# Kernel tuning notes

Measured on AMD Instinct MI355X. Metric: run time of the kernel, lower is better.

## Reference

```python
import jax, jax.numpy as jnp
import numpy as np

RADIUS = 0.1
NSAMPLE = 32


def _ball_query(radius, nsample, xyz, new_xyz):
    # xyz: (B,N,3), new_xyz: (B,npoint,3) -> idx (B,npoint,nsample) int32
    # Faithful to the CUDA ball_query: take the first nsample in-radius indices
    # (in ascending point order); pad with the first found index.
    N = xyz.shape[1]
    d2 = jnp.sum((new_xyz[:, :, None, :] - xyz[:, None, :, :]) ** 2, axis=-1)  # (B,np,N)
    mask = d2 < radius * radius
    key_arr = jnp.where(mask, jnp.arange(N, dtype=jnp.int32), jnp.int32(N))
    idx = jnp.sort(key_arr, axis=-1)[..., :nsample]  # (B,np,ns)
    first = idx[..., :1]
    idx = jnp.where(idx == N, first, idx)
    idx = jnp.where(idx == N, 0, idx)  # empty-ball fallback (matches zero-init buffer)
    return idx


def _group(features, idx):
    # features (B,C,N), idx (B,np,ns) -> (B,C,np,ns)
    return jax.vmap(lambda f, i: f[:, i])(features, idx)


def _forward(xyz, new_xyz):
    idx = jax.lax.stop_gradient(_ball_query(RADIUS, NSAMPLE, xyz, new_xyz))
    xyz_t = jnp.transpose(xyz, (0, 2, 1))                 # (B,3,N)
    g = _group(xyz_t, idx)                                # (B,3,np,ns) grouped_xyz
    c = jnp.transpose(new_xyz, (0, 2, 1))[..., None]      # (B,3,np,1)  new_xyz_reshaped

    # pairwise distances within each group
    diff = g[..., :, None] - g[..., None, :]              # (B,3,np,ns,ns)
    dis = jnp.sqrt(jnp.sum(diff * diff, axis=1))          # (B,np,ns,ns)
    mean_dis = jnp.mean(dis, axis=3)                      # (B,np,ns)
    tip_idx = jnp.argmax(mean_dis, axis=2)                # (B,np)
    tip_pts = jnp.take_along_axis(g, tip_idx[:, None, :, None], axis=3)[..., 0]  # (B,3,np)

    cb = jnp.broadcast_to(c, g.shape)                     # (B,3,np,ns)
    gpv = jnp.cross(jnp.cross(cb, g, axis=1), cb, axis=1)
    gpv = gpv / jnp.linalg.norm(gpv, axis=1)[:, None]     # (B,3,np,ns)

    new_r = jnp.sqrt(jnp.sum(c * c, axis=1))              # (B,np,1)
    new_norm = c / (new_r[:, None] + 1e-8)                # (B,3,np,1)

    c3 = c[..., 0]                                        # (B,3,np)
    tpv = jnp.cross(jnp.cross(c3, tip_pts, axis=1), c3, axis=1)
    tpv = tpv / jnp.linalg.norm(tpv, axis=1)[:, None]     # (B,3,np)

    gcv = jnp.cross(gpv, jnp.broadcast_to(tpv[..., None], gpv.shape), axis=1)
    sinv = jnp.sum(gcv * new_norm, axis=1)                # (B,np,ns)

    dis_t = jnp.transpose(dis, (0, 2, 1, 3))              # (B,ns,np,ns)
    dis_sort = jnp.sort(dis_t, axis=1) * sinv[:, None]    # (B,ns,np,ns)
    grouped_r = jnp.sqrt(jnp.sum(g * g, axis=1))          # (B,np,ns)
    return jnp.concatenate([dis_sort, grouped_r[:, None]], axis=1)  # (B,ns+1,np,ns)


def setup_inputs() -> dict:
    key = jax.random.key(0)
    k1, k2 = jax.random.split(key)
    xyz = jax.random.uniform(k1, (4, 16384, 3), dtype=jnp.float32)
    new_xyz = jax.random.uniform(k2, (4, 2048, 3), dtype=jnp.float32)
    return {"xyz": xyz, "new_xyz": new_xyz}


def reference(xyz, new_xyz):
    return _forward(xyz, new_xyz)
```

## Files before the change

kernel.cpp:

```cpp
#include <hip/hip_runtime.h>


#define BB 4
#define NN 16384
#define MM 2048
#define NS 32
#define R2 0.01f
#define NCELL 1000
#define CPAD 1024
#define HCAP 128

#define WS_PTS_OFF (16 * 1024)
#define WS_NEED (WS_PTS_OFF + (size_t)BB * NN * 16)

__device__ __forceinline__ int cell_of(float x, float y, float z) {
    int ci = (int)(x * 10.0f); ci = ci < 0 ? 0 : (ci > 9 ? 9 : ci);
    int cj = (int)(y * 10.0f); cj = cj < 0 ? 0 : (cj > 9 ? 9 : cj);
    int ck = (int)(z * 10.0f); ck = ck < 0 ? 0 : (ck > 9 ? 9 : ck);
    return (ci * 10 + cj) * 10 + ck;
}

__global__ __launch_bounds__(1024) void k_build(const float* __restrict__ xyz,
                                                int* __restrict__ off,
                                                float4* __restrict__ pts) {
    __shared__ int sc[1024];
    __shared__ int wsum[16];
    const int b = blockIdx.x, t = threadIdx.x;
    const int lane = t & 63, wid = t >> 6;
    sc[t] = 0;
    __syncthreads();
    const float* xp = xyz + (size_t)b * NN * 3;
    float X[16], Y[16], Z[16]; int C[16];
    #pragma unroll
    for (int k = 0; k < 16; ++k) {
        int i = k * 1024 + t;
        const float* p = xp + (size_t)i * 3;
        X[k] = p[0]; Y[k] = p[1]; Z[k] = p[2];
        C[k] = cell_of(X[k], Y[k], Z[k]);
        atomicAdd(&sc[C[k]], 1);
    }
    __syncthreads();
    int v = sc[t];
    int x = v;
    #pragma unroll
    for (int o = 1; o < 64; o <<= 1) {
        int u = __shfl_up(x, o);
        if (lane >= o) x += u;
    }
    if (lane == 63) wsum[wid] = x;
    __syncthreads();
    int pre = 0;
    #pragma unroll
    for (int i2 = 0; i2 < 16; ++i2) pre += (i2 < wid) ? wsum[i2] : 0;
    int incl = x + pre;
    int excl = incl - v;
    if (t < NCELL) off[b * CPAD + t] = excl;
    if (t == 1023) off[b * CPAD + NCELL] = incl;
    __syncthreads();
    sc[t] = excl;
    __syncthreads();
    #pragma unroll
    for (int k = 0; k < 16; ++k) {
        int pos = atomicAdd(&sc[C[k]], 1);
        int i = k * 1024 + t;
        pts[(size_t)b * NN + pos] = make_float4(X[k], Y[k], Z[k], __int_as_float(i));
    }
}

__global__ __launch_bounds__(256) void qgr_grid_kernel(
    const float* __restrict__ xyz,
    const float* __restrict__ nxyz,
    const int* __restrict__ offi,
    const float4* __restrict__ pts,
    float* __restrict__ out) {

    __shared__ float s_hx[4][2][HCAP], s_hy[4][2][HCAP], s_hz[4][2][HCAP];
    __shared__ int   s_hidx[4][2][HCAP];

    const int lane = threadIdx.x & 63;
    const int w = threadIdx.x >> 6;
    const int sub = lane & 31;
    const int half = lane >> 5;
    const int q0 = blockIdx.x * 8 + w * 2;
    const int b = q0 >> 11;

    const float* xb = xyz + (size_t)b * NN * 3;
    const float* nq = nxyz + (size_t)q0 * 3;
    const float cx0 = nq[0], cy0 = nq[1], cz0 = nq[2];
    const float cx1 = nq[3], cy1 = nq[4], cz1 = nq[5];
    const unsigned long long lmask = (1ull << lane) - 1ull;

    const int* offb = offi + b * CPAD;
    const float4* ptsb = pts + (size_t)b * NN;

    int hits01[2];
    for (int tq = 0; tq < 2; ++tq) {
        const float ccx = tq ? cx1 : cx0;
        const float ccy = tq ? cy1 : cy0;
        const float ccz = tq ? cz1 : cz0;

        int ci0 = (int)(ccx * 10.0f); ci0 = ci0 < 0 ? 0 : (ci0 > 9 ? 9 : ci0);
        int cj0 = (int)(ccy * 10.0f); cj0 = cj0 < 0 ? 0 : (cj0 > 9 ? 9 : cj0);
        int ck0 = (int)(ccz * 10.0f); ck0 = ck0 < 0 ? 0 : (ck0 > 9 ? 9 : ck0);
        int zlo = ck0 > 0 ? ck0 - 1 : 0;
        int zhi = ck0 < 9 ? ck0 + 1 : 9;

        int rs[9], rl[9];
        #pragma unroll
        for (int r = 0; r < 9; ++r) { rs[r] = 0; rl[r] = 0; }
        int nr = 0;
        #pragma unroll
        for (int di = -1; di <= 1; ++di) {
            int ii = ci0 + di; if ((unsigned)ii > 9u) continue;
            #pragma unroll
            for (int dj = -1; dj <= 1; ++dj) {
                int jj = cj0 + dj; if ((unsigned)jj > 9u) continue;
                int base2 = (ii * 10 + jj) * 10;
                int s0 = offb[base2 + zlo];
                int e0 = offb[base2 + zhi + 1];
                int len = e0 - s0;
                if (len > 0) { rs[nr] = s0; rl[nr] = len; ++nr; }
            }
        }

        float4 P[9];
        #pragma unroll
        for (int r = 0; r < 9; ++r) {
            int a = (lane < rl[r]) ? (rs[r] + lane) : 0;
            P[r] = ptsb[a];
        }

        int hits = 0;
        #pragma unroll
        for (int r = 0; r < 9; ++r) {
            float dx = __fsub_rn(ccx, P[r].x);
            float dy = __fsub_rn(ccy, P[r].y);
            float dz = __fsub_rn(ccz, P[r].z);
            float d2 = __fadd_rn(__fadd_rn(__fmul_rn(dx, dx), __fmul_rn(dy, dy)),
                                 __fmul_rn(dz, dz));
            bool hit = (lane < rl[r]) && (d2 < R2);
            unsigned long long bal = __ballot(hit);
            if (bal) {
                int rank = __popcll(bal & lmask);
                int slot = hits + rank;
                if (hit && slot < HCAP) {
                    s_hx[w][tq][slot] = P[r].x; s_hy[w][tq][slot] = P[r].y;
                    s_hz[w][tq][slot] = P[r].z; s_hidx[w][tq][slot] = __float_as_int(P[r].w);
                }
                hits += __popcll(bal);
            }
        }
        for (int r = 0; r < nr; ++r) {
            for (int t0 = 64; t0 < rl[r]; t0 += 64) {
                int t = t0 + lane;
                bool act = t < rl[r];
                float4 Q = ptsb[rs[r] + (act ? t : 0)];
                float dx = __fsub_rn(ccx, Q.x);
                float dy = __fsub_rn(ccy, Q.y);
                float dz = __fsub_rn(ccz, Q.z);
                float d2 = __fadd_rn(__fadd_rn(__fmul_rn(dx, dx), __fmul_rn(dy, dy)),
                                     __fmul_rn(dz, dz));
                bool hit = act && (d2 < R2);
                unsigned long long bal = __ballot(hit);
                if (bal) {
                    int rank = __popcll(bal & lmask);
                    int slot = hits + rank;
                    if (hit && slot < HCAP) {
                        s_hx[w][tq][slot] = Q.x; s_hy[w][tq][slot] = Q.y;
                        s_hz[w][tq][slot] = Q.z; s_hidx[w][tq][slot] = __float_as_int(Q.w);
                    }
                    hits += __popcll(bal);
                }
            }
        }
        hits01[tq] = hits;
    }

    const int hits = half ? hits01[1] : hits01[0];
    const int cap = hits < HCAP ? hits : HCAP;
    const float ccx = half ? cx1 : cx0;
    const float ccy = half ? cy1 : cy0;
    const float ccz = half ? cz1 : cz0;

    int key[4];
    #pragma unroll
    for (int r = 0; r < 4; ++r) {
        int e = r * 32 + sub;
        key[r] = (e < cap) ? ((s_hidx[w][half][e] << 8) | e) : 0x7fffffff;
    }

    #pragma unroll
    for (int k = 2; k <= 16; k <<= 1) {
        #pragma unroll
        for (int j = k >> 1; j > 0; j >>= 1) {
            bool lower = (sub & j) == 0;
            bool asc = (sub & k) == 0;
            bool keepmin = (lower == asc);
            #pragma unroll
            for (int r = 0; r < 4; ++r) {
                int p = __shfl_xor(key[r], j);
                key[r] = keepmin ? min(key[r], p) : max(key[r], p);
            }
        }
    }
    #pragma unroll
    for (int j = 16; j > 0; j >>= 1) {
        bool lower = (sub & j) == 0;
        #pragma unroll
        for (int r = 0; r < 4; ++r) {
            int p = __shfl_xor(key[r], j);
            bool asc = (r & 1) == 0;
            key[r] = (lower == asc) ? min(key[r], p) : max(key[r], p);
        }
    }
    {
        int t0 = min(key[0], key[1]); key[1] = max(key[0], key[1]); key[0] = t0;
        int t2 = max(key[2], key[3]); key[3] = min(key[2], key[3]); key[2] = t2;
    }
    #pragma unroll
    for (int j = 16; j > 0; j >>= 1) {
        bool lower = (sub & j) == 0;
        #pragma unroll
        for (int r = 0; r < 4; ++r) {
            int p = __shfl_xor(key[r], j);
            bool asc = (r & 2) == 0;
            key[r] = (lower == asc) ? min(key[r], p) : max(key[r], p);
        }
    }
    {
        int t0 = min(key[0], key[2]); key[2] = max(key[0], key[2]); key[0] = t0;
        int t1 = min(key[1], key[3]); key[3] = max(key[1], key[3]); key[1] = t1;
        t0 = min(key[0], key[1]); key[1] = max(key[0], key[1]); key[0] = t0;
        t1 = min(key[2], key[3]); key[3] = max(key[2], key[3]); key[2] = t1;
    }
    #pragma unroll
    for (int j = 16; j > 0; j >>= 1) {
        bool lower = (sub & j) == 0;
        #pragma unroll
        for (int r = 0; r < 4; ++r) {
            int p = __shfl_xor(key[r], j);
            key[r] = lower ? min(key[r], p) : max(key[r], p);
        }
    }

    const int found = hits < NS ? hits : NS;
    const int hbase = half << 5;
    float hx = 0.f, hy = 0.f, hz = 0.f;
    if (sub < found) {
        int s = key[0] & 0xFF;
        hx = s_hx[w][half][s]; hy = s_hy[w][half][s]; hz = s_hz[w][half][s];
    }
    float p0x, p0y, p0z;
    if (found == 0) { p0x = xb[0]; p0y = xb[1]; p0z = xb[2]; }
    else { p0x = __shfl(hx, hbase); p0y = __shfl(hy, hbase); p0z = __shfl(hz, hbase); }
    if (sub >= found) { hx = p0x; hy = p0y; hz = p0z; }

    float v[NS];
    #pragma unroll
    for (int ii = 0; ii < NS; ++ii) {
        float bx = __shfl(hx, hbase + ii);
        float by = __shfl(hy, hbase + ii);
        float bz = __shfl(hz, hbase + ii);
        float dx = __fsub_rn(bx, hx);
        float dy = __fsub_rn(by, hy);
        float dz = __fsub_rn(bz, hz);
        v[ii] = sqrtf(__fadd_rn(__fadd_rn(__fmul_rn(dx, dx), __fmul_rn(dy, dy)),
                                __fmul_rn(dz, dz)));
    }

    float r8[8];
    #pragma unroll
    for (int t = 0; t < 8; ++t) {
        r8[t] = __fadd_rn(__fadd_rn(__fadd_rn(v[t], v[t + 8]), v[t + 16]), v[t + 24]);
    }
    float mv = __fadd_rn(__fadd_rn(__fadd_rn(r8[0], r8[1]), __fadd_rn(r8[2], r8[3])),
                         __fadd_rn(__fadd_rn(r8[4], r8[5]), __fadd_rn(r8[6], r8[7])));
    int mi = sub;
    #pragma unroll
    for (int off = 1; off < 32; off <<= 1) {
        float ov = __shfl_xor(mv, off);
        int oi = __shfl_xor(mi, off);
        if (ov > mv || (ov == mv && oi < mi)) { mv = ov; mi = oi; }
    }

    float tx = __shfl(hx, hbase + mi), ty = __shfl(hy, hbase + mi), tz = __shfl(hz, hbase + mi);

    float ux = ccy * tz - ccz * ty, uy = ccz * tx - ccx * tz, uz = ccx * ty - ccy * tx;
    float vx = uy * ccz - uz * ccy, vy = uz * ccx - ux * ccz, vz = ux * ccy - uy * ccx;
    float vn = fmaxf(sqrtf(vx * vx + vy * vy + vz * vz), 1e-37f);
    float tnx = vx / vn, tny = vy / vn, tnz = vz / vn;

    float nrm = sqrtf(ccx * ccx + ccy * ccy + ccz * ccz);
    float dn = nrm + 1e-8f;
    float nnx = ccx / dn, nny = ccy / dn, nnz = ccz / dn;

    float ax = ccy * hz - ccz * hy, ay = ccz * hx - ccx * hz, az = ccx * hy - ccy * hx;
    float px = ay * ccz - az * ccy, py = az * ccx - ax * ccz, pz = ax * ccy - ay * ccx;
    float pn = fmaxf(sqrtf(px * px + py * py + pz * pz), 1e-37f);
    px /= pn; py /= pn; pz /= pn;

    float qx = py * tnz - pz * tny;
    float qy = pz * tnx - px * tnz;
    float qz = px * tny - py * tnx;
    float sinv = qx * nnx + qy * nny + qz * nnz;

    float gr = sqrtf(hx * hx + hy * hy + hz * hz);

    const int m_h = (q0 + half) & (MM - 1);
    const size_t rowstride = (size_t)MM * NS;
    const size_t obase = (((size_t)b * 33) * MM + m_h) * NS + sub;
    out[obase + 32 * rowstride] = gr;

    #pragma unroll
    for (int k = 2; k <= NS; k <<= 1) {
        #pragma unroll
        for (int jj = k >> 1; jj > 0; jj >>= 1) {
            #pragma unroll
            for (int ii = 0; ii < NS; ++ii) {
                int ll = ii ^ jj;
                if (ll > ii) {
                    bool up = ((ii & k) == 0);
                    float a = v[ii], c2 = v[ll];
                    bool sw = up ? (a > c2) : (a < c2);
                    if (sw) { v[ii] = c2; v[ll] = a; }
                }
            }
        }
    }

    #pragma unroll
    for (int ii = 0; ii < NS; ++ii)
        out[obase + (size_t)ii * rowstride] = v[ii] * sinv;
}

#define CHUNKS 4
__global__ __launch_bounds__(256) void qgr_kernel(
    const float* __restrict__ xyz,
    const float* __restrict__ nxyz,
    float* __restrict__ out) {

    __shared__ float s_gx[4][NS], s_gy[4][NS], s_gz[4][NS];
    __shared__ float s_dis[4][NS][NS + 1];

    const int lane = threadIdx.x & 63;
    const int w = threadIdx.x >> 6;
    const int q = blockIdx.x * 4 + w;
    const int b = q >> 11;
    const int m = q & (MM - 1);

    const float* xb = xyz + (size_t)b * NN * 3;
    const float* nq = nxyz + (size_t)q * 3;
    const float cx = nq[0], cy = nq[1], cz = nq[2];
    const unsigned long long lmask = (1ull << lane) - 1ull;

    int cnt = 0;
    for (int base = 0; base < NN; base += 64 * CHUNKS) {
        float X[CHUNKS], Y[CHUNKS], Z[CHUNKS];
        #pragma unroll
        for (int c = 0; c < CHUNKS; ++c) {
            const float* p = xb + (size_t)(base + c * 64 + lane) * 3;
            X[c] = p[0]; Y[c] = p[1]; Z[c] = p[2];
        }
        bool in[CHUNKS];
        #pragma unroll
        for (int c = 0; c < CHUNKS; ++c) {
            float dx = __fsub_rn(cx, X[c]);
            float dy = __fsub_rn(cy, Y[c]);
            float dz = __fsub_rn(cz, Z[c]);
            float d2 = __fadd_rn(__fadd_rn(__fmul_rn(dx, dx), __fmul_rn(dy, dy)),
                                 __fmul_rn(dz, dz));
            in[c] = d2 < R2;
        }
        #pragma unroll
        for (int c = 0; c < CHUNKS; ++c) {
            unsigned long long bal = __ballot(in[c]);
            if (bal) {
                int rank = __popcll(bal & lmask);
                int slot = cnt + rank;
                if (in[c] && slot < NS) {
                    s_gx[w][slot] = X[c]; s_gy[w][slot] = Y[c]; s_gz[w][slot] = Z[c];
                }
                cnt += __popcll(bal);
            }
        }
        if (cnt >= NS) break;
    }
    __syncthreads();

    int found = cnt < NS ? cnt : NS;
    float p0x, p0y, p0z;
    if (found == 0) { p0x = xb[0]; p0y = xb[1]; p0z = xb[2]; }
    else            { p0x = s_gx[w][0]; p0y = s_gy[w][0]; p0z = s_gz[w][0]; }
    if (lane < NS && lane >= found) {
        s_gx[w][lane] = p0x; s_gy[w][lane] = p0y; s_gz[w][lane] = p0z;
    }
    __syncthreads();

    #pragma unroll
    for (int t = 0; t < 16; ++t) {
        int e = t * 64 + lane;
        int di = e >> 5, dj = e & 31;
        float dx = __fsub_rn(s_gx[w][di], s_gx[w][dj]);
        float dy = __fsub_rn(s_gy[w][di], s_gy[w][dj]);
        float dz = __fsub_rn(s_gz[w][di], s_gz[w][dj]);
        s_dis[w][di][dj] =
            sqrtf(__fadd_rn(__fadd_rn(__fmul_rn(dx, dx), __fmul_rn(dy, dy)), __fmul_rn(dz, dz)));
    }
    __syncthreads();

    {
        int i = lane & 31;
        float r[8];
        #pragma unroll
        for (int t = 0; t < 8; ++t) {
            r[t] = __fadd_rn(__fadd_rn(__fadd_rn(s_dis[w][i][t], s_dis[w][i][t + 8]),
                                        s_dis[w][i][t + 16]),
                             s_dis[w][i][t + 24]);
        }
        float mv = __fadd_rn(__fadd_rn(__fadd_rn(r[0], r[1]), __fadd_rn(r[2], r[3])),
                             __fadd_rn(__fadd_rn(r[4], r[5]), __fadd_rn(r[6], r[7])));
        int mi = i;
        #pragma unroll
        for (int off = 1; off < 64; off <<= 1) {
            float ov = __shfl_xor(mv, off);
            int oi = __shfl_xor(mi, off);
            if (ov > mv || (ov == mv && oi < mi)) { mv = ov; mi = oi; }
        }
        float tx = s_gx[w][mi], ty = s_gy[w][mi], tz = s_gz[w][mi];
        float ux = cy * tz - cz * ty, uy = cz * tx - cx * tz, uz = cx * ty - cy * tx;
        float vx = uy * cz - uz * cy, vy = uz * cx - ux * cz, vz = ux * cy - uy * cx;
        float vn = fmaxf(sqrtf(vx * vx + vy * vy + vz * vz), 1e-37f);
        float tnx = vx / vn, tny = vy / vn, tnz = vz / vn;
        float nr = sqrtf(cx * cx + cy * cy + cz * cz);
        float dn = nr + 1e-8f;
        float nnx = cx / dn, nny = cy / dn, nnz = cz / dn;
        int j = lane & 31;
        float gx = s_gx[w][j], gy = s_gy[w][j], gz = s_gz[w][j];
        float ax = cy * gz - cz * gy, ay = cz * gx - cx * gz, az = cx * gy - cy * gx;
        float px = ay * cz - az * cy, py = az * cx - ax * cz, pz = ax * cy - ay * cx;
        float pn = fmaxf(sqrtf(px * px + py * py + pz * pz), 1e-37f);
        px /= pn; py /= pn; pz /= pn;
        float qx = py * tnz - pz * tny;
        float qy = pz * tnx - px * tnz;
        float qz = px * tny - py * tnx;
        float sinv = qx * nnx + qy * nny + qz * nnz;
        float gr = sqrtf(gx * gx + gy * gy + gz * gz);
        const size_t rowstride = (size_t)MM * NS;
        const size_t obase = (((size_t)b * 33) * MM + m) * NS + j;
        if (lane < NS) out[obase + 32 * rowstride] = gr;
        float v[NS];
        #pragma unroll
        for (int ii = 0; ii < NS; ++ii) v[ii] = s_dis[w][ii][j];
        #pragma unroll
        for (int k = 2; k <= NS; k <<= 1) {
            #pragma unroll
            for (int jj = k >> 1; jj > 0; jj >>= 1) {
                #pragma unroll
                for (int ii = 0; ii < NS; ++ii) {
                    int ll = ii ^ jj;
                    if (ll > ii) {
                        bool up = ((ii & k) == 0);
                        float a = v[ii], c2 = v[ll];
                        bool sw = up ? (a > c2) : (a < c2);
                        if (sw) { v[ii] = c2; v[ll] = a; }
                    }
                }
            }
        }
        if (lane < NS) {
            #pragma unroll
            for (int ii = 0; ii < NS; ++ii)
                out[obase + (size_t)ii * rowstride] = v[ii] * sinv;
        }
    }
}

extern "C" void kernel_launch(void* const* d_in, const int* in_sizes, int n_in,
                              void* d_out, int out_size, void* d_ws, size_t ws_size,
                              hipStream_t stream) {
    (void)in_sizes; (void)n_in; (void)out_size;
    const float* xyz = (const float*)d_in[0];
    const float* nxyz = (const float*)d_in[1];
    float* out = (float*)d_out;

    if (d_ws != nullptr && ws_size >= WS_NEED) {
        char* ws = (char*)d_ws;
        int* off = (int*)ws;
        float4* pts = (float4*)(ws + WS_PTS_OFF);
        k_build<<<BB, 1024, 0, stream>>>(xyz, off, pts);
        qgr_grid_kernel<<<(BB * MM) / 8, 256, 0, stream>>>(xyz, nxyz, off, pts, out);
    } else {
        qgr_kernel<<<(BB * MM) / 4, 256, 0, stream>>>(xyz, nxyz, out);
    }
}
```

Baseline: 105.3 us.

## Refine grid z-resolution, pack hits as float4, use LDS broadcast and odd-even merge sort

Doubles the grid resolution along z (20 cells) and scans a 5-cell z window, which shrinks the candidate set per query. Hit buffers become float4 arrays so each hit is stored and gathered with one wide access. Per-lane point broadcasts move from shuffles to LDS reads. The bitonic sort of the per-lane distances is replaced by Batcher odd-even merge sort built from fminf/fmaxf, which needs fewer compare-exchanges. The new layout uses more LDS and a slightly larger offset table.

```diff
diff --git a/kernel.cpp b/kernel.cpp
--- a/kernel.cpp
+++ b/kernel.cpp
@@ -6,28 +6,29 @@
 #define MM 2048
 #define NS 32
 #define R2 0.01f
-#define NCELL 1000
-#define CPAD 1024
+#define GZ 20
+#define NCELL 2000
+#define CPAD 2048
 #define HCAP 128
 
-#define WS_PTS_OFF (16 * 1024)
+#define WS_PTS_OFF (32 * 1024)
 #define WS_NEED (WS_PTS_OFF + (size_t)BB * NN * 16)
 
 __device__ __forceinline__ int cell_of(float x, float y, float z) {
     int ci = (int)(x * 10.0f); ci = ci < 0 ? 0 : (ci > 9 ? 9 : ci);
     int cj = (int)(y * 10.0f); cj = cj < 0 ? 0 : (cj > 9 ? 9 : cj);
-    int ck = (int)(z * 10.0f); ck = ck < 0 ? 0 : (ck > 9 ? 9 : ck);
-    return (ci * 10 + cj) * 10 + ck;
+    int ck = (int)(z * 20.0f); ck = ck < 0 ? 0 : (ck > 19 ? 19 : ck);
+    return (ci * 10 + cj) * GZ + ck;
 }
 
 __global__ __launch_bounds__(1024) void k_build(const float* __restrict__ xyz,
                                                 int* __restrict__ off,
                                                 float4* __restrict__ pts) {
-    __shared__ int sc[1024];
+    __shared__ int sc[CPAD];
     __shared__ int wsum[16];
     const int b = blockIdx.x, t = threadIdx.x;
     const int lane = t & 63, wid = t >> 6;
-    sc[t] = 0;
+    sc[t] = 0; sc[1024 + t] = 0;
     __syncthreads();
     const float* xp = xyz + (size_t)b * NN * 3;
     float X[16], Y[16], Z[16]; int C[16];
@@ -40,8 +41,9 @@
         atomicAdd(&sc[C[k]], 1);
     }
     __syncthreads();
-    int v = sc[t];
-    int x = v;
+    int v0 = sc[2 * t], v1 = sc[2 * t + 1];
+    int s = v0 + v1;
+    int x = s;
     #pragma unroll
     for (int o = 1; o < 64; o <<= 1) {
         int u = __shfl_up(x, o);
@@ -53,11 +55,11 @@
     #pragma unroll
     for (int i2 = 0; i2 < 16; ++i2) pre += (i2 < wid) ? wsum[i2] : 0;
     int incl = x + pre;
-    int excl = incl - v;
-    if (t < NCELL) off[b * CPAD + t] = excl;
-    if (t == 1023) off[b * CPAD + NCELL] = incl;
-    __syncthreads();
-    sc[t] = excl;
+    int excl = incl - s;
+    off[b * CPAD + 2 * t] = excl;
+    off[b * CPAD + 2 * t + 1] = excl + v0;
+    __syncthreads();
+    sc[2 * t] = excl; sc[2 * t + 1] = excl + v0;
     __syncthreads();
     #pragma unroll
     for (int k = 0; k < 16; ++k) {
@@ -74,8 +76,8 @@
     const float4* __restrict__ pts,
     float* __restrict__ out) {
 
-    __shared__ float s_hx[4][2][HCAP], s_hy[4][2][HCAP], s_hz[4][2][HCAP];
-    __shared__ int   s_hidx[4][2][HCAP];
+    __shared__ float4 s_hit[4][2][HCAP];
+    __shared__ float4 s_sel[4][2][NS];
 
     const int lane = threadIdx.x & 63;
     const int w = threadIdx.x >> 6;
@@ -101,9 +103,9 @@
 
         int ci0 = (int)(ccx * 10.0f); ci0 = ci0 < 0 ? 0 : (ci0 > 9 ? 9 : ci0);
         int cj0 = (int)(ccy * 10.0f); cj0 = cj0 < 0 ? 0 : (cj0 > 9 ? 9 : cj0);
-        int ck0 = (int)(ccz * 10.0f); ck0 = ck0 < 0 ? 0 : (ck0 > 9 ? 9 : ck0);
-        int zlo = ck0 > 0 ? ck0 - 1 : 0;
-        int zhi = ck0 < 9 ? ck0 + 1 : 9;
+        int ck0 = (int)(ccz * 20.0f); ck0 = ck0 < 0 ? 0 : (ck0 > 19 ? 19 : ck0);
+        int zlo = ck0 > 2 ? ck0 - 2 : 0;
+        int zhi = ck0 < 17 ? ck0 + 2 : 19;
 
         int rs[9], rl[9];
         #pragma unroll
@@ -115,7 +117,7 @@
             #pragma unroll
             for (int dj = -1; dj <= 1; ++dj) {
                 int jj = cj0 + dj; if ((unsigned)jj > 9u) continue;
-                int base2 = (ii * 10 + jj) * 10;
+                int base2 = (ii * 10 + jj) * GZ;
                 int s0 = offb[base2 + zlo];
                 int e0 = offb[base2 + zhi + 1];
                 int len = e0 - s0;
@@ -143,10 +145,7 @@
             if (bal) {
                 int rank = __popcll(bal & lmask);
                 int slot = hits + rank;
-                if (hit && slot < HCAP) {
-                    s_hx[w][tq][slot] = P[r].x; s_hy[w][tq][slot] = P[r].y;
-                    s_hz[w][tq][slot] = P[r].z; s_hidx[w][tq][slot] = __float_as_int(P[r].w);
-                }
+                if (hit && slot < HCAP) s_hit[w][tq][slot] = P[r];
                 hits += __popcll(bal);
             }
         }
@@ -165,10 +164,7 @@
                 if (bal) {
                     int rank = __popcll(bal & lmask);
                     int slot = hits + rank;
-                    if (hit && slot < HCAP) {
-                        s_hx[w][tq][slot] = Q.x; s_hy[w][tq][slot] = Q.y;
-                        s_hz[w][tq][slot] = Q.z; s_hidx[w][tq][slot] = __float_as_int(Q.w);
-                    }
+                    if (hit && slot < HCAP) s_hit[w][tq][slot] = Q;
                     hits += __popcll(bal);
                 }
             }
@@ -186,7 +182,8 @@
     #pragma unroll
     for (int r = 0; r < 4; ++r) {
         int e = r * 32 + sub;
-        key[r] = (e < cap) ? ((s_hidx[w][half][e] << 8) | e) : 0x7fffffff;
+        int idx_e = __float_as_int(s_hit[w][half][e].w);
+        key[r] = (e < cap) ? ((idx_e << 8) | e) : 0x7fffffff;
     }
 
     #pragma unroll
@@ -245,25 +242,25 @@
 
     const int found = hits < NS ? hits : NS;
     const int hbase = half << 5;
-    float hx = 0.f, hy = 0.f, hz = 0.f;
-    if (sub < found) {
-        int s = key[0] & 0xFF;
-        hx = s_hx[w][half][s]; hy = s_hy[w][half][s]; hz = s_hz[w][half][s];
-    }
+    float4 sel = make_float4(0.f, 0.f, 0.f, 0.f);
+    if (sub < found) sel = s_hit[w][half][key[0] & 0xFF];
     float p0x, p0y, p0z;
     if (found == 0) { p0x = xb[0]; p0y = xb[1]; p0z = xb[2]; }
-    else { p0x = __shfl(hx, hbase); p0y = __shfl(hy, hbase); p0z = __shfl(hz, hbase); }
-    if (sub >= found) { hx = p0x; hy = p0y; hz = p0z; }
+    else {
+        p0x = __shfl(sel.x, hbase); p0y = __shfl(sel.y, hbase); p0z = __shfl(sel.z, hbase);
+    }
+    if (sub >= found) { sel.x = p0x; sel.y = p0y; sel.z = p0z; }
+    const float hx = sel.x, hy = sel.y, hz = sel.z;
+
+    s_sel[w][half][sub] = sel;
 
     float v[NS];
     #pragma unroll
     for (int ii = 0; ii < NS; ++ii) {
-        float bx = __shfl(hx, hbase + ii);
-        float by = __shfl(hy, hbase + ii);
-        float bz = __shfl(hz, hbase + ii);
-        float dx = __fsub_rn(bx, hx);
-        float dy = __fsub_rn(by, hy);
-        float dz = __fsub_rn(bz, hz);
+        float4 B = s_sel[w][half][ii];
+        float dx = __fsub_rn(B.x, hx);
+        float dy = __fsub_rn(B.y, hy);
+        float dz = __fsub_rn(B.z, hz);
         v[ii] = sqrtf(__fadd_rn(__fadd_rn(__fmul_rn(dx, dx), __fmul_rn(dy, dy)),
                                 __fmul_rn(dz, dz)));
     }
@@ -283,7 +280,8 @@
         if (ov > mv || (ov == mv && oi < mi)) { mv = ov; mi = oi; }
     }
 
-    float tx = __shfl(hx, hbase + mi), ty = __shfl(hy, hbase + mi), tz = __shfl(hz, hbase + mi);
+    float4 T = s_sel[w][half][mi];
+    const float tx = T.x, ty = T.y, tz = T.z;
 
     float ux = ccy * tz - ccz * ty, uy = ccz * tx - ccx * tz, uz = ccx * ty - ccy * tx;
     float vx = uy * ccz - uz * ccy, vy = uz * ccx - ux * ccz, vz = ux * ccy - uy * ccx;
@@ -312,17 +310,21 @@
     out[obase + 32 * rowstride] = gr;
 
     #pragma unroll
-    for (int k = 2; k <= NS; k <<= 1) {
-        #pragma unroll
-        for (int jj = k >> 1; jj > 0; jj >>= 1) {
+    for (int p = 1; p < NS; p <<= 1) {
+        #pragma unroll
+        for (int k = p; k >= 1; k >>= 1) {
             #pragma unroll
-            for (int ii = 0; ii < NS; ++ii) {
-                int ll = ii ^ jj;
-                if (ll > ii) {
-                    bool up = ((ii & k) == 0);
-                    float a = v[ii], c2 = v[ll];
-                    bool sw = up ? (a > c2) : (a < c2);
-                    if (sw) { v[ii] = c2; v[ll] = a; }
+            for (int j = k & (p - 1); j + k < NS; j += 2 * k) {
+                #pragma unroll
+                for (int i = 0; i < k; ++i) {
+                    if (i + j + k < NS) {
+                        int x = i + j, y = i + j + k;
+                        if ((x / (2 * p)) == (y / (2 * p))) {
+                            float lo = fminf(v[x], v[y]);
+                            v[y] = fmaxf(v[x], v[y]);
+                            v[x] = lo;
+                        }
+                    }
                 }
             }
         }
```

New measurement: 103.4 us. About the same (-1.8%).
